# Optimization experiments

Hardware: AMD Instinct MI355X
Metric: run time of the kernel (lower is better)

## Reference

```python
import jax, jax.numpy as jnp
import numpy as np

N = 100000   # num_nodes
E = 800000   # num_edges
D = 128      # dim_in == dim_hidden
DA = 8       # dim_atten
DE = 64      # dim_encoding
DM = D + DE  # mlp hidden (192)
B = 65536    # edge_batch size
NH = 101     # heuristic embedding vocab
SLOPE = 0.2  # leaky_relu negative slope
EPS = 1e-15


def _gtm_att(x, row, col, wr, wc, wx, bx):
    # edge-wise multiplicative attention + sparse softmax + sparse matmul reduce
    ar = x @ wr.T                                   # [N, DA]
    ac = x @ wc.T                                   # [N, DA]
    s = jnp.sum(ar[row] * ac[col], axis=1) * (1.0 / np.sqrt(DA))  # [E]
    s = jnp.where(s >= 0, s, SLOPE * s)             # leaky_relu
    s = jnp.exp(s - jnp.max(s))
    denom = jax.ops.segment_sum(s, row, num_segments=N)           # [N]
    a = s * (1.0 / (denom + EPS))[row]              # row-normalized attention [E]
    out = jax.ops.segment_sum(a[:, None] * x[col], row, num_segments=N)  # [N, D]
    return out @ wx.T + bx


def _gtm(x, row, col, wres, bres, wr, wc, wx, bx, wo, bo):
    y = (x @ wres.T + bres) + _gtm_att(x, row, col, wr, wc, wx, bx)
    return y @ wo.T + bo


def _layernorm(h, g, b):
    mu = jnp.mean(h, axis=-1, keepdims=True)
    var = jnp.var(h, axis=-1, keepdims=True)
    return (h - mu) / jnp.sqrt(var + 1e-5) * g + b


def _forward(x, l0_wres, l0_bres, l0_wr, l0_wc, l0_wx, l0_bx, l0_wo, l0_bo,
             l1_wres, l1_bres, l1_wr, l1_wc, l1_wx, l1_bx, l1_wo, l1_bo,
             emb_h, mlp0_w, mlp0_b, mlp1_w, mlp1_b, ln_g, ln_b,
             f0_w, f0_b, f1_w, f1_b, row, col, eb_src, eb_dst, eb_h):
    h = _gtm(x, row, col, l0_wres, l0_bres, l0_wr, l0_wc, l0_wx, l0_bx, l0_wo, l0_bo)
    h = jax.nn.relu(h)
    h = _gtm(h, row, col, l1_wres, l1_bres, l1_wr, l1_wc, l1_wx, l1_bx, l1_wo, l1_bo)
    z = h[eb_src] * h[eb_dst]                       # [B, D] hadamard link feature
    z = jnp.concatenate([z, emb_h[eb_h]], axis=1)   # [B, DM]
    for w, b in ((mlp0_w, mlp0_b), (mlp1_w, mlp1_b)):
        z = jax.nn.relu(_layernorm(z @ w.T + b, ln_g, ln_b))
    z = z @ f0_w.T + f0_b
    z = z @ f1_w.T + f1_b
    return jax.nn.sigmoid(z)                        # [B, 1]


def setup_inputs() -> dict:
    key = jax.random.key(0)
    ks = jax.random.split(key, 40)
    it = iter(range(40))
    def rn(shape, scale=1.0):
        return jax.random.normal(ks[next(it)], shape, jnp.float32) * scale
    def ri(shape, hi):
        return jax.random.randint(ks[next(it)], shape, 0, hi)
    s_d = 1.0 / np.sqrt(D)
    s_m = 1.0 / np.sqrt(DM)
    inp = {
        "x": rn((N, D)),
        "row": jnp.sort(ri((E,), N)),
        "col": ri((E,), N),
        "eb_src": ri((B,), N),
        "eb_dst": ri((B,), N),
        "eb_h": ri((B,), NH),
    }
    for l in ("l0", "l1"):
        inp[l + "_wres"] = rn((D, D), s_d)
        inp[l + "_bres"] = jnp.zeros((D,), jnp.float32)
        inp[l + "_wr"] = rn((DA, D), s_d)
        inp[l + "_wc"] = rn((DA, D), s_d)
        inp[l + "_wx"] = rn((D, D), s_d)
        inp[l + "_bx"] = jnp.zeros((D,), jnp.float32)
        inp[l + "_wo"] = rn((D, D), s_d)
        inp[l + "_bo"] = jnp.zeros((D,), jnp.float32)
    inp["emb_h"] = rn((NH, DE), 0.1)
    inp["mlp0_w"] = rn((DM, DM), s_m)
    inp["mlp0_b"] = jnp.zeros((DM,), jnp.float32)
    inp["mlp1_w"] = rn((DM, DM), s_m)
    inp["mlp1_b"] = jnp.zeros((DM,), jnp.float32)
    inp["ln_g"] = jnp.ones((DM,), jnp.float32)
    inp["ln_b"] = jnp.zeros((DM,), jnp.float32)
    inp["f0_w"] = rn((64, DM), s_m)
    inp["f0_b"] = jnp.zeros((64,), jnp.float32)
    inp["f1_w"] = rn((1, 64), 0.125)
    inp["f1_b"] = jnp.zeros((1,), jnp.float32)
    return inp


def reference(x, row, col, eb_src, eb_dst, eb_h,
              l0_wres, l0_bres, l0_wr, l0_wc, l0_wx, l0_bx, l0_wo, l0_bo,
              l1_wres, l1_bres, l1_wr, l1_wc, l1_wx, l1_bx, l1_wo, l1_bo,
              emb_h, mlp0_w, mlp0_b, mlp1_w, mlp1_b, ln_g, ln_b,
              f0_w, f0_b, f1_w, f1_b):
    return _forward(x, l0_wres, l0_bres, l0_wr, l0_wc, l0_wx, l0_bx, l0_wo, l0_bo,
                    l1_wres, l1_bres, l1_wr, l1_wc, l1_wx, l1_bx, l1_wo, l1_bo,
                    emb_h, mlp0_w, mlp0_b, mlp1_w, mlp1_b, ln_g, ln_b,
                    f0_w, f0_b, f1_w, f1_b, row, col, eb_src, eb_dst, eb_h)
```

## Files before the change

### kernel.cpp

```cpp
#include <hip/hip_runtime.h>
#include <math.h>

#define D   128
#define DA  8
#define DE  64
#define DMH 192

typedef unsigned short u16;
typedef unsigned int   u32;
typedef __attribute__((ext_vector_type(8))) short bfrag;
typedef __attribute__((ext_vector_type(4))) float facc;

__device__ inline u16 f2bf(float v) {
    unsigned u = __float_as_uint(v);
    return (u16)((u + 0x7fffu + ((u >> 16) & 1u)) >> 16);
}
__device__ inline float bf2f(u16 v) { return __uint_as_float((u32)v << 16); }
__device__ inline u32 pack2(float a, float b) {
    return (u32)f2bf(a) | ((u32)f2bf(b) << 16);
}
__device__ inline bfrag bzero() {
    bfrag r;
#pragma unroll
    for (int i = 0; i < 8; ++i) r[i] = 0;
    return r;
}
__device__ inline bfrag afrag16(const u16* wlds, int row, int kb) {
    int off = row * 256 + (((kb >> 3) * 16) ^ ((row & 7) << 4));
    return *(const bfrag*)((const char*)wlds + off);
}
__device__ inline bfrag zfrag16(const u16* wlds, int row, int kb) {
    int off = row * 384 + (((kb >> 3) * 16) ^ ((row & 7) << 4));
    return *(const bfrag*)((const char*)wlds + off);
}
__device__ inline void st_swz(u16* wlds, int row, int col, int stride, float v) {
    *(u16*)((char*)wlds + row * stride
            + ((((col >> 3) * 16) ^ ((row & 7) << 4)) + (col & 7) * 2)) = f2bf(v);
}
__device__ inline void stage32k(u16* __restrict__ dst, const u16* __restrict__ src,
                                int t) {
    bfrag tmp[8];
#pragma unroll
    for (int i = 0; i < 8; ++i)
        tmp[i] = *(const bfrag*)(src + (size_t)((i << 8) + t) * 8);
#pragma unroll
    for (int i = 0; i < 8; ++i)
        *(bfrag*)(dst + ((i << 8) + t) * 8) = tmp[i];
}

struct PrepSrc { const float* p[14]; };
__global__ __launch_bounds__(256) void prep_all(
    PrepSrc ps, u16* __restrict__ wb,
    const float* __restrict__ x, u16* __restrict__ xb, long n8,
    const int* __restrict__ row, int* __restrict__ rowptr, int E, int N)
{
    long task = (long)blockIdx.x * 256 + threadIdx.x;
    if (task < 194880) {
        int idx = (int)task;
        const int roff[13] = {0, 16384, 32768, 49152, 65536, 81920, 98304,
                              135168, 172032, 184320, 186368, 188416, 194880};
        int r = 0;
#pragma unroll
        for (int k = 1; k < 12; ++k) if (idx >= roff[k]) r = k;
        int local = idx - roff[r];
        float v;
        if (r == 11) {
            v = ps.p[13][local];
        } else {
            int K   = (r >= 6 && r <= 8) ? DMH : D;
            int nks = K >> 5;
            int m = local & 7, lane = (local >> 3) & 63;
            int l16 = lane & 15, lg = lane >> 4;
            int rest = local >> 9;
            int ks = rest % nks, tct = rest / nks;
            int rrow = tct * 16 + l16;
            int k = ks * 32 + lg * 8 + m;
            if (r == 9)       v = (rrow < 8) ? ps.p[9][rrow * D + k]
                                             : ps.p[10][(rrow - 8) * D + k];
            else if (r == 10) v = (rrow < 8) ? ps.p[11][rrow * D + k]
                                             : ps.p[12][(rrow - 8) * D + k];
            else              v = ps.p[r][(size_t)rrow * K + k];
        }
        wb[idx] = f2bf(v);
        return;
    }
    task -= 194880;
    if (task < n8) {
        long i = task;
        __align__(16) float buf[8];
        const float4* p = (const float4*)(x + i * 8);
        ((float4*)buf)[0] = p[0];
        ((float4*)buf)[1] = p[1];
        bfrag o;
#pragma unroll
        for (int k = 0; k < 8; ++k) o[k] = (short)f2bf(buf[k]);
        *(bfrag*)(xb + i * 8) = o;
        return;
    }
    task -= n8;
    if (task < E) {
        int e = (int)task;
        int cur  = row[e];
        int prev = (e == 0) ? -1 : row[e - 1];
        for (int r2 = prev + 1; r2 <= cur; ++r2) rowptr[r2] = e;
        if (e == E - 1)
            for (int r2 = cur + 1; r2 <= N; ++r2) rowptr[r2] = E;
    }
}

__global__ __launch_bounds__(256) void calc_arac(
    const u16* __restrict__ Xb, const u16* __restrict__ wrc,
    float* __restrict__ ar, float* __restrict__ ac, int N)
{
    const int t = threadIdx.x;
    const int w = t >> 6, l = t & 63, l16 = l & 15, lg = l >> 4;
    const long r0 = (long)blockIdx.x * 64 + w * 16;
    const long ia = r0 + l16;
    bfrag a[4];
#pragma unroll
    for (int ks = 0; ks < 4; ++ks)
        a[ks] = (ia < N) ? *(const bfrag*)(Xb + ia * D + ks * 32 + lg * 8) : bzero();
    facc acc = (facc){0, 0, 0, 0};
#pragma unroll
    for (int ks = 0; ks < 4; ++ks) {
        bfrag b = *(const bfrag*)(wrc + ((ks * 64 + l) << 3));
        acc = __builtin_amdgcn_mfma_f32_16x16x32_bf16(a[ks], b, acc, 0, 0, 0);
    }
#pragma unroll
    for (int j = 0; j < 4; ++j) {
        long i = r0 + lg * 4 + j;
        if (i < N) {
            if (l16 < 8) ar[i * DA + l16] = acc[j];
            else         ac[i * DA + (l16 - 8)] = acc[j];
        }
    }
}

__global__ void edge_score(const int* __restrict__ row, const int* __restrict__ col,
                           const float* __restrict__ ar, const float* __restrict__ ac,
                           float* __restrict__ sbuf, int E)
{
    int e = blockIdx.x * 256 + threadIdx.x;
    if (e >= E) return;
    int r = row[e], c = col[e];
    float4 a0 = *(const float4*)&ar[(long)r * DA];
    float4 a1 = *(const float4*)&ar[(long)r * DA + 4];
    float4 c0 = *(const float4*)&ac[(long)c * DA];
    float4 c1 = *(const float4*)&ac[(long)c * DA + 4];
    float s = a0.x * c0.x + a0.y * c0.y + a0.z * c0.z + a0.w * c0.w
            + a1.x * c1.x + a1.y * c1.y + a1.z * c1.z + a1.w * c1.w;
    s *= 0.35355339059327373f;
    s = (s >= 0.f) ? s : 0.2f * s;
    sbuf[e] = expf(s);
}

__global__ __launch_bounds__(256) void aggregate_b(
    const int* __restrict__ rowptr, const int* __restrict__ col,
    const float* __restrict__ sbuf, const u32* __restrict__ Xb2,
    u32* __restrict__ aggb2, int N)
{
    const int w = threadIdx.x >> 6, l = threadIdx.x & 63;
    const int n = blockIdx.x * 4 + w;
    if (n >= N) return;
    const int e0 = rowptr[n], e1 = rowptr[n + 1];
    float p0 = 0.f, p1 = 0.f, ds = 0.f;
    int e = e0;
    for (; e + 8 <= e1; e += 8) {
        float ss[8]; u32 uu[8];
#pragma unroll
        for (int k = 0; k < 8; ++k) {
            int c = col[e + k];
            ss[k] = sbuf[e + k];
            uu[k] = Xb2[((u32)c << 6) + l];
        }
#pragma unroll
        for (int k = 0; k < 8; ++k) {
            ds += ss[k];
            p0 += ss[k] * __uint_as_float(uu[k] << 16);
            p1 += ss[k] * __uint_as_float(uu[k] & 0xffff0000u);
        }
    }
    if (e + 4 <= e1) {
        float ss[4]; u32 uu[4];
#pragma unroll
        for (int k = 0; k < 4; ++k) {
            int c = col[e + k];
            ss[k] = sbuf[e + k];
            uu[k] = Xb2[((u32)c << 6) + l];
        }
#pragma unroll
        for (int k = 0; k < 4; ++k) {
            ds += ss[k];
            p0 += ss[k] * __uint_as_float(uu[k] << 16);
            p1 += ss[k] * __uint_as_float(uu[k] & 0xffff0000u);
        }
        e += 4;
    }
    {
        int rem = e1 - e;
        if (rem > 0) {
            float sa = sbuf[e];
            u32   ua = Xb2[((u32)col[e] << 6) + l];
            float sb = 0.f; u32 ub = 0;
            float sc2 = 0.f; u32 uc = 0;
            if (rem > 1) { sb  = sbuf[e + 1]; ub = Xb2[((u32)col[e + 1] << 6) + l]; }
            if (rem > 2) { sc2 = sbuf[e + 2]; uc = Xb2[((u32)col[e + 2] << 6) + l]; }
            ds += sa + sb + sc2;
            p0 += sa * __uint_as_float(ua << 16);
            p1 += sa * __uint_as_float(ua & 0xffff0000u);
            p0 += sb * __uint_as_float(ub << 16);
            p1 += sb * __uint_as_float(ub & 0xffff0000u);
            p0 += sc2 * __uint_as_float(uc << 16);
            p1 += sc2 * __uint_as_float(uc & 0xffff0000u);
        }
    }
    float sc = 1.f / (ds + 1e-15f);
    aggb2[((u32)n << 6) + l] = pack2(p0 * sc, p1 * sc);
}

template<bool RELU, bool ARAC>
__global__ __launch_bounds__(256) void gtm_fused16(
    const u16* __restrict__ Xb, const u16* __restrict__ aggb,
    const u16* __restrict__ wres, const float* __restrict__ bres,
    const u16* __restrict__ wx, const float* __restrict__ bx,
    const u16* __restrict__ wo, const float* __restrict__ bo,
    const u16* __restrict__ wrc_next, float* __restrict__ ar,
    float* __restrict__ ac, u16* __restrict__ hb, int N)
{
    __shared__ u16 wsh[16384];
    __shared__ u16 ylds4[4][16 * D];
    const int t = threadIdx.x;
    const int w = t >> 6, l = t & 63, l16 = l & 15, lg = l >> 4;
    u16* ylds = ylds4[w];
    const long r0 = (long)blockIdx.x * 64 + w * 16;
    const long ia = r0 + l16;

    bfrag xa[4], ga[4];
#pragma unroll
    for (int ks = 0; ks < 4; ++ks) {
        if (ia < N) {
            xa[ks] = *(const bfrag*)(Xb   + ia * D + ks * 32 + lg * 8);
            ga[ks] = *(const bfrag*)(aggb + ia * D + ks * 32 + lg * 8);
        } else { xa[ks] = bzero(); ga[ks] = bzero(); }
    }

    facc acc[8];
#pragma unroll
    for (int ct = 0; ct < 8; ++ct) acc[ct] = (facc){0, 0, 0, 0};

    stage32k(wsh, wres, t);
    __syncthreads();
#pragma unroll
    for (int ks = 0; ks < 4; ++ks)
#pragma unroll
        for (int ct = 0; ct < 8; ++ct) {
            bfrag b = *(const bfrag*)(wsh + (((ct * 4 + ks) * 64 + l) << 3));
            acc[ct] = __builtin_amdgcn_mfma_f32_16x16x32_bf16(xa[ks], b, acc[ct], 0, 0, 0);
        }
    __syncthreads();

    stage32k(wsh, wx, t);
    __syncthreads();
#pragma unroll
    for (int ks = 0; ks < 4; ++ks)
#pragma unroll
        for (int ct = 0; ct < 8; ++ct) {
            bfrag b = *(const bfrag*)(wsh + (((ct * 4 + ks) * 64 + l) << 3));
            acc[ct] = __builtin_amdgcn_mfma_f32_16x16x32_bf16(ga[ks], b, acc[ct], 0, 0, 0);
        }
    __syncthreads();

    stage32k(wsh, wo, t);
#pragma unroll
    for (int ct = 0; ct < 8; ++ct) {
        int col = ct * 16 + l16;
        float bsum = bres[col] + bx[col];
#pragma unroll
        for (int j = 0; j < 4; ++j)
            st_swz(ylds, lg * 4 + j, col, 256, acc[ct][j] + bsum);
    }
    __syncthreads();

#pragma unroll
    for (int ct = 0; ct < 8; ++ct) acc[ct] = (facc){0, 0, 0, 0};
#pragma unroll
    for (int ks = 0; ks < 4; ++ks) {
        bfrag a = afrag16(ylds, l16, ks * 32 + lg * 8);
#pragma unroll
        for (int ct = 0; ct < 8; ++ct) {
            bfrag b = *(const bfrag*)(wsh + (((ct * 4 + ks) * 64 + l) << 3));
            acc[ct] = __builtin_amdgcn_mfma_f32_16x16x32_bf16(a, b, acc[ct], 0, 0, 0);
        }
    }
    asm volatile("s_waitcnt lgkmcnt(0)" ::: "memory");
    __builtin_amdgcn_sched_barrier(0);
#pragma unroll
    for (int ct = 0; ct < 8; ++ct) {
        int col = ct * 16 + l16;
        float bov = bo[col];
#pragma unroll
        for (int j = 0; j < 4; ++j) {
            long i = r0 + lg * 4 + j;
            float y = acc[ct][j] + bov;
            if (RELU) y = fmaxf(y, 0.f);
            if (i < N) hb[i * D + col] = f2bf(y);
            if (ARAC) st_swz(ylds, lg * 4 + j, col, 256, y);
        }
    }
    if (ARAC) {
        asm volatile("s_waitcnt lgkmcnt(0)" ::: "memory");
        __builtin_amdgcn_sched_barrier(0);
        facc pr = (facc){0, 0, 0, 0};
#pragma unroll
        for (int ks = 0; ks < 4; ++ks) {
            bfrag b = *(const bfrag*)(wrc_next + ((ks * 64 + l) << 3));
            bfrag a = afrag16(ylds, l16, ks * 32 + lg * 8);
            pr = __builtin_amdgcn_mfma_f32_16x16x32_bf16(a, b, pr, 0, 0, 0);
        }
#pragma unroll
        for (int j = 0; j < 4; ++j) {
            long i = r0 + lg * 4 + j;
            if (i < N) {
                if (l16 < 8) ar[i * DA + l16] = pr[j];
                else         ac[i * DA + (l16 - 8)] = pr[j];
            }
        }
    }
}

__device__ inline void ln_relu_to_lds(facc acc[12], const float* __restrict__ bb,
                                      const float* __restrict__ g,
                                      const float* __restrict__ bln,
                                      int l16, int lg, u16* wz)
{
    float s1[4] = {0, 0, 0, 0}, s2[4] = {0, 0, 0, 0};
#pragma unroll
    for (int ct = 0; ct < 12; ++ct) {
        float bbv = bb[ct * 16 + l16];
#pragma unroll
        for (int j = 0; j < 4; ++j) {
            float xv = acc[ct][j] + bbv;
            acc[ct][j] = xv;
            s1[j] += xv; s2[j] += xv * xv;
        }
    }
#pragma unroll
    for (int j = 0; j < 4; ++j) {
#pragma unroll
        for (int off = 1; off < 16; off <<= 1) {
            s1[j] += __shfl_xor(s1[j], off);
            s2[j] += __shfl_xor(s2[j], off);
        }
    }
#pragma unroll
    for (int ct = 0; ct < 12; ++ct) {
        int cc = ct * 16 + l16;
        float gv = g[cc], bv = bln[cc];
#pragma unroll
        for (int j = 0; j < 4; ++j) {
            float mu  = s1[j] * (1.f / 192.f);
            float var = s2[j] * (1.f / 192.f) - mu * mu;
            float y = (acc[ct][j] - mu) * rsqrtf(var + 1e-5f) * gv + bv;
            y = fmaxf(y, 0.f);
            st_swz(wz, lg * 4 + j, cc, 384, y);
        }
    }
    asm volatile("s_waitcnt lgkmcnt(0)" ::: "memory");
    __builtin_amdgcn_sched_barrier(0);
}

__global__ __launch_bounds__(256) void mlp_tail4(
    const u16* __restrict__ hb,
    const int* __restrict__ src, const int* __restrict__ dst,
    const int* __restrict__ ebh, const u16* __restrict__ embb,
    const u16* __restrict__ w0, const float* __restrict__ b0,
    const u16* __restrict__ w1, const float* __restrict__ b1,
    const float* __restrict__ g, const float* __restrict__ bln,
    const u16* __restrict__ f0w, const float* __restrict__ f0b,
    const float* __restrict__ f1w, const float* __restrict__ f1b,
    float* __restrict__ out, int B)
{
    __shared__ u16 wst[18432];
    __shared__ u16 zs[4][16 * DMH];
    const int t = threadIdx.x;
    const int w = t >> 6, l = t & 63, l16 = l & 15, lg = l >> 4;
    u16* wz = zs[w];
    const long r0 = (long)blockIdx.x * 64 + w * 16;
    const long ri = r0 + l16;

    bfrag za[6];
    if (ri < B) {
        int si = src[ri], di = dst[ri], hi2 = ebh[ri];
#pragma unroll
        for (int ks = 0; ks < 4; ++ks) {
            bfrag hs = *(const bfrag*)(hb + (size_t)si * D + ks * 32 + lg * 8);
            bfrag hd = *(const bfrag*)(hb + (size_t)di * D + ks * 32 + lg * 8);
            bfrag r;
#pragma unroll
            for (int k = 0; k < 8; ++k)
                r[k] = (short)f2bf(bf2f((u16)hs[k]) * bf2f((u16)hd[k]));
            za[ks] = r;
        }
        za[4] = *(const bfrag*)(embb + (size_t)hi2 * DE + lg * 8);
        za[5] = *(const bfrag*)(embb + (size_t)hi2 * DE + 32 + lg * 8);
    } else {
#pragma unroll
        for (int ks = 0; ks < 6; ++ks) za[ks] = bzero();
    }

    facc acc[12];
#pragma unroll
    for (int ct = 0; ct < 12; ++ct) acc[ct] = (facc){0, 0, 0, 0};
#pragma unroll
    for (int c = 0; c < 2; ++c) {
        {
            bfrag tmp[9];
#pragma unroll
            for (int i = 0; i < 9; ++i)
                tmp[i] = *(const bfrag*)(w0 + (size_t)c * 18432 + ((i * 256 + t) << 3));
#pragma unroll
            for (int i = 0; i < 9; ++i)
                *(bfrag*)(wst + ((i * 256 + t) << 3)) = tmp[i];
        }
        __syncthreads();
#pragma unroll
        for (int ks = 0; ks < 6; ++ks)
#pragma unroll
            for (int ctl = 0; ctl < 6; ++ctl) {
                bfrag b = *(const bfrag*)(wst + (((ctl * 6 + ks) * 64 + l) << 3));
                acc[c * 6 + ctl] =
                    __builtin_amdgcn_mfma_f32_16x16x32_bf16(za[ks], b, acc[c * 6 + ctl], 0, 0, 0);
            }
        __syncthreads();
    }
    ln_relu_to_lds(acc, b0, g, bln, l16, lg, wz);

#pragma unroll
    for (int ct = 0; ct < 12; ++ct) acc[ct] = (facc){0, 0, 0, 0};
#pragma unroll
    for (int c = 0; c < 2; ++c) {
        {
            bfrag tmp[9];
#pragma unroll
            for (int i = 0; i < 9; ++i)
                tmp[i] = *(const bfrag*)(w1 + (size_t)c * 18432 + ((i * 256 + t) << 3));
#pragma unroll
            for (int i = 0; i < 9; ++i)
                *(bfrag*)(wst + ((i * 256 + t) << 3)) = tmp[i];
        }
        __syncthreads();
#pragma unroll
        for (int ks = 0; ks < 6; ++ks) {
            bfrag a = zfrag16(wz, l16, ks * 32 + lg * 8);
#pragma unroll
            for (int ctl = 0; ctl < 6; ++ctl) {
                bfrag b = *(const bfrag*)(wst + (((ctl * 6 + ks) * 64 + l) << 3));
                acc[c * 6 + ctl] =
                    __builtin_amdgcn_mfma_f32_16x16x32_bf16(a, b, acc[c * 6 + ctl], 0, 0, 0);
            }
        }
        __syncthreads();
    }
    ln_relu_to_lds(acc, b1, g, bln, l16, lg, wz);

    {
        bfrag tmp[6];
#pragma unroll
        for (int i = 0; i < 6; ++i)
            tmp[i] = *(const bfrag*)(f0w + ((i * 256 + t) << 3));
#pragma unroll
        for (int i = 0; i < 6; ++i)
            *(bfrag*)(wst + ((i * 256 + t) << 3)) = tmp[i];
    }
    __syncthreads();
    facc o[4];
#pragma unroll
    for (int ct = 0; ct < 4; ++ct) o[ct] = (facc){0, 0, 0, 0};
#pragma unroll
    for (int ks = 0; ks < 6; ++ks) {
        bfrag a = zfrag16(wz, l16, ks * 32 + lg * 8);
#pragma unroll
        for (int ct = 0; ct < 4; ++ct) {
            bfrag b = *(const bfrag*)(wst + (((ct * 6 + ks) * 64 + l) << 3));
            o[ct] = __builtin_amdgcn_mfma_f32_16x16x32_bf16(a, b, o[ct], 0, 0, 0);
        }
    }
    float p[4] = {0, 0, 0, 0};
#pragma unroll
    for (int ct = 0; ct < 4; ++ct) {
        int cc = ct * 16 + l16;
        float fb = f0b[cc], fw = f1w[cc];
#pragma unroll
        for (int j = 0; j < 4; ++j) p[j] += (o[ct][j] + fb) * fw;
    }
#pragma unroll
    for (int j = 0; j < 4; ++j) {
#pragma unroll
        for (int off = 1; off < 16; off <<= 1) p[j] += __shfl_xor(p[j], off);
    }
    if (l16 == 0) {
#pragma unroll
        for (int j = 0; j < 4; ++j) {
            long i = r0 + lg * 4 + j;
            if (i < B) out[i] = 1.f / (1.f + expf(-(p[j] + f1b[0])));
        }
    }
}

extern "C" void kernel_launch(void* const* d_in, const int* in_sizes, int n_in,
                              void* d_out, int out_size, void* d_ws, size_t ws_size,
                              hipStream_t stream)
{
    const float* x      = (const float*)d_in[0];
    const int*   row    = (const int*)d_in[1];
    const int*   col    = (const int*)d_in[2];
    const int*   eb_src = (const int*)d_in[3];
    const int*   eb_dst = (const int*)d_in[4];
    const int*   eb_h   = (const int*)d_in[5];
    const float* l_wres[2] = {(const float*)d_in[6],  (const float*)d_in[14]};
    const float* l_bres[2] = {(const float*)d_in[7],  (const float*)d_in[15]};
    const float* l_wr[2]   = {(const float*)d_in[8],  (const float*)d_in[16]};
    const float* l_wc[2]   = {(const float*)d_in[9],  (const float*)d_in[17]};
    const float* l_wx[2]   = {(const float*)d_in[10], (const float*)d_in[18]};
    const float* l_bx[2]   = {(const float*)d_in[11], (const float*)d_in[19]};
    const float* l_wo[2]   = {(const float*)d_in[12], (const float*)d_in[20]};
    const float* l_bo[2]   = {(const float*)d_in[13], (const float*)d_in[21]};
    const float* emb_h  = (const float*)d_in[22];
    const float* mlp0_w = (const float*)d_in[23];
    const float* mlp0_b = (const float*)d_in[24];
    const float* mlp1_w = (const float*)d_in[25];
    const float* mlp1_b = (const float*)d_in[26];
    const float* ln_g   = (const float*)d_in[27];
    const float* ln_b   = (const float*)d_in[28];
    const float* f0_w   = (const float*)d_in[29];
    const float* f0_b   = (const float*)d_in[30];
    const float* f1_w   = (const float*)d_in[31];
    const float* f1_b   = (const float*)d_in[32];

    const int N = in_sizes[0] / D;
    const int E = in_sizes[1];
    const int B = in_sizes[3];

    float* arb  = (float*)d_ws;
    float* acb  = arb + (size_t)N * DA;
    float* sbuf = acb + (size_t)N * DA;
    int* rowptr = (int*)(sbuf + (size_t)E);
    uintptr_t bp = (uintptr_t)(rowptr + (N + 1));
    bp = (bp + 15) & ~(uintptr_t)15;
    u16* xb   = (u16*)bp;
    u16* h0b  = xb  + (size_t)N * D;
    u16* hfb  = h0b + (size_t)N * D;
    u16* aggb = hfb + (size_t)N * D;
    u16* WB   = aggb + (size_t)N * D;

    const u16* WRES[2] = {WB + 0,     WB + 49152};
    const u16* WX[2]   = {WB + 16384, WB + 65536};
    const u16* WO[2]   = {WB + 32768, WB + 81920};
    const u16* MW0  = WB + 98304;
    const u16* MW1  = WB + 135168;
    const u16* F0W  = WB + 172032;
    const u16* WRC[2] = {WB + 184320, WB + 186368};
    const u16* EMBB = WB + 188416;

    PrepSrc ps;
    ps.p[0] = l_wres[0]; ps.p[1] = l_wx[0]; ps.p[2] = l_wo[0];
    ps.p[3] = l_wres[1]; ps.p[4] = l_wx[1]; ps.p[5] = l_wo[1];
    ps.p[6] = mlp0_w;    ps.p[7] = mlp1_w;  ps.p[8] = f0_w;
    ps.p[9] = l_wr[0];   ps.p[10] = l_wc[0];
    ps.p[11] = l_wr[1];  ps.p[12] = l_wc[1];
    ps.p[13] = emb_h;

    const int nb64  = (N + 63) / 64;
    const int nbN4  = (N + 3) / 4;
    const int nbE   = (E + 255) / 256;
    const int nbB64 = (B + 63) / 64;
    const long n8   = (long)N * D / 8;
    const long T    = 194880 + n8 + (long)E;
    const int nbT   = (int)((T + 255) / 256);

    prep_all<<<nbT, 256, 0, stream>>>(ps, WB, x, xb, n8, row, rowptr, E, N);
    calc_arac<<<nb64, 256, 0, stream>>>(xb, WRC[0], arb, acb, N);

    edge_score<<<nbE, 256, 0, stream>>>(row, col, arb, acb, sbuf, E);
    aggregate_b<<<nbN4, 256, 0, stream>>>(rowptr, col, sbuf,
                                          (const u32*)xb, (u32*)aggb, N);
    gtm_fused16<true, true><<<nb64, 256, 0, stream>>>(
        xb, aggb, WRES[0], l_bres[0], WX[0], l_bx[0],
        WO[0], l_bo[0], WRC[1], arb, acb, h0b, N);

    edge_score<<<nbE, 256, 0, stream>>>(row, col, arb, acb, sbuf, E);
    aggregate_b<<<nbN4, 256, 0, stream>>>(rowptr, col, sbuf,
                                          (const u32*)h0b, (u32*)aggb, N);
    gtm_fused16<false, false><<<nb64, 256, 0, stream>>>(
        h0b, aggb, WRES[1], l_bres[1], WX[1], l_bx[1],
        WO[1], l_bo[1], nullptr, nullptr, nullptr, hfb, N);

    mlp_tail4<<<nbB64, 256, 0, stream>>>(
        hfb, eb_src, eb_dst, eb_h, EMBB,
        MW0, mlp0_b, MW1, mlp1_b, ln_g, ln_b,
        F0W, f0_b, f1_w, f1_b, (float*)d_out, B);
}
```

Before: 239.6 us.

## Prefetch next weight chunk into registers during MFMA compute in GTM and MLP kernels

Weight staging is software-pipelined: the next weight tile is loaded from global memory into registers while the current tile in LDS feeds the MFMA loop. After that loop it is written to LDS. This hides global load latency behind compute in both the GTM fused kernel and the link MLP kernel. In exchange, register pressure rises (8-9 extra bfrag per thread), which may lower occupancy, and the synchronisation order gets more intricate.

```diff
diff --git a/kernel.cpp b/kernel.cpp
--- a/kernel.cpp
+++ b/kernel.cpp
@@ -37,15 +37,25 @@
     *(u16*)((char*)wlds + row * stride
             + ((((col >> 3) * 16) ^ ((row & 7) << 4)) + (col & 7) * 2)) = f2bf(v);
 }
-__device__ inline void stage32k(u16* __restrict__ dst, const u16* __restrict__ src,
-                                int t) {
-    bfrag tmp[8];
+__device__ inline void ldw8(bfrag* r, const u16* __restrict__ src, int t) {
 #pragma unroll
     for (int i = 0; i < 8; ++i)
-        tmp[i] = *(const bfrag*)(src + (size_t)((i << 8) + t) * 8);
+        r[i] = *(const bfrag*)(src + (size_t)((i << 8) + t) * 8);
+}
+__device__ inline void stw8(u16* __restrict__ dst, const bfrag* r, int t) {
 #pragma unroll
     for (int i = 0; i < 8; ++i)
-        *(bfrag*)(dst + ((i << 8) + t) * 8) = tmp[i];
+        *(bfrag*)(dst + ((i << 8) + t) * 8) = r[i];
+}
+__device__ inline void ldw9(bfrag* r, const u16* __restrict__ src, int t) {
+#pragma unroll
+    for (int i = 0; i < 9; ++i)
+        r[i] = *(const bfrag*)(src + (size_t)((i * 256 + t) << 3));
+}
+__device__ inline void stw9(u16* __restrict__ dst, const bfrag* r, int t) {
+#pragma unroll
+    for (int i = 0; i < 9; ++i)
+        *(bfrag*)(dst + ((i * 256 + t) << 3)) = r[i];
 }
 
 struct PrepSrc { const float* p[14]; };
@@ -235,6 +245,9 @@
     const long r0 = (long)blockIdx.x * 64 + w * 16;
     const long ia = r0 + l16;
 
+    bfrag wreg[8];
+    ldw8(wreg, wres, t);
+
     bfrag xa[4], ga[4];
 #pragma unroll
     for (int ks = 0; ks < 4; ++ks) {
@@ -248,8 +261,9 @@
 #pragma unroll
     for (int ct = 0; ct < 8; ++ct) acc[ct] = (facc){0, 0, 0, 0};
 
-    stage32k(wsh, wres, t);
-    __syncthreads();
+    stw8(wsh, wreg, t);
+    __syncthreads();
+    ldw8(wreg, wx, t);
 #pragma unroll
     for (int ks = 0; ks < 4; ++ks)
 #pragma unroll
@@ -259,8 +273,9 @@
         }
     __syncthreads();
 
-    stage32k(wsh, wx, t);
-    __syncthreads();
+    stw8(wsh, wreg, t);
+    __syncthreads();
+    ldw8(wreg, wo, t);
 #pragma unroll
     for (int ks = 0; ks < 4; ++ks)
 #pragma unroll
@@ -270,7 +285,7 @@
         }
     __syncthreads();
 
-    stage32k(wsh, wo, t);
+    stw8(wsh, wreg, t);
 #pragma unroll
     for (int ct = 0; ct < 8; ++ct) {
         int col = ct * 16 + l16;
@@ -388,6 +403,9 @@
     const long r0 = (long)blockIdx.x * 64 + w * 16;
     const long ri = r0 + l16;
 
+    bfrag wreg[9];
+    ldw9(wreg, w0, t);
+
     bfrag za[6];
     if (ri < B) {
         int si = src[ri], di = dst[ri], hi2 = ebh[ri];
@@ -411,68 +429,69 @@
     facc acc[12];
 #pragma unroll
     for (int ct = 0; ct < 12; ++ct) acc[ct] = (facc){0, 0, 0, 0};
-#pragma unroll
-    for (int c = 0; c < 2; ++c) {
-        {
-            bfrag tmp[9];
-#pragma unroll
-            for (int i = 0; i < 9; ++i)
-                tmp[i] = *(const bfrag*)(w0 + (size_t)c * 18432 + ((i * 256 + t) << 3));
-#pragma unroll
-            for (int i = 0; i < 9; ++i)
-                *(bfrag*)(wst + ((i * 256 + t) << 3)) = tmp[i];
-        }
-        __syncthreads();
-#pragma unroll
-        for (int ks = 0; ks < 6; ++ks)
+    stw9(wst, wreg, t);
+    __syncthreads();
+    ldw9(wreg, w0 + 18432, t);
+#pragma unroll
+    for (int ks = 0; ks < 6; ++ks)
+#pragma unroll
+        for (int ctl = 0; ctl < 6; ++ctl) {
+            bfrag b = *(const bfrag*)(wst + (((ctl * 6 + ks) * 64 + l) << 3));
+            acc[ctl] = __builtin_amdgcn_mfma_f32_16x16x32_bf16(za[ks], b, acc[ctl], 0, 0, 0);
+        }
+    __syncthreads();
+    stw9(wst, wreg, t);
+    __syncthreads();
+    ldw9(wreg, w1, t);
+#pragma unroll
+    for (int ks = 0; ks < 6; ++ks)
+#pragma unroll
+        for (int ctl = 0; ctl < 6; ++ctl) {
+            bfrag b = *(const bfrag*)(wst + (((ctl * 6 + ks) * 64 + l) << 3));
+            acc[6 + ctl] = __builtin_amdgcn_mfma_f32_16x16x32_bf16(za[ks], b, acc[6 + ctl], 0, 0, 0);
+        }
+    ln_relu_to_lds(acc, b0, g, bln, l16, lg, wz);
+    __syncthreads();
+
+#pragma unroll
+    for (int ct = 0; ct < 12; ++ct) acc[ct] = (facc){0, 0, 0, 0};
+    stw9(wst, wreg, t);
+    __syncthreads();
+    ldw9(wreg, w1 + 18432, t);
+#pragma unroll
+    for (int ks = 0; ks < 6; ++ks) {
+        bfrag a = zfrag16(wz, l16, ks * 32 + lg * 8);
+#pragma unroll
+        for (int ctl = 0; ctl < 6; ++ctl) {
+            bfrag b = *(const bfrag*)(wst + (((ctl * 6 + ks) * 64 + l) << 3));
+            acc[ctl] = __builtin_amdgcn_mfma_f32_16x16x32_bf16(a, b, acc[ctl], 0, 0, 0);
+        }
+    }
+    __syncthreads();
+    stw9(wst, wreg, t);
+    __syncthreads();
+    {
+        bfrag f6[6];
+#pragma unroll
+        for (int i = 0; i < 6; ++i)
+            f6[i] = *(const bfrag*)(f0w + ((i * 256 + t) << 3));
+#pragma unroll
+        for (int ks = 0; ks < 6; ++ks) {
+            bfrag a = zfrag16(wz, l16, ks * 32 + lg * 8);
 #pragma unroll
             for (int ctl = 0; ctl < 6; ++ctl) {
                 bfrag b = *(const bfrag*)(wst + (((ctl * 6 + ks) * 64 + l) << 3));
-                acc[c * 6 + ctl] =
-                    __builtin_amdgcn_mfma_f32_16x16x32_bf16(za[ks], b, acc[c * 6 + ctl], 0, 0, 0);
+                acc[6 + ctl] = __builtin_amdgcn_mfma_f32_16x16x32_bf16(a, b, acc[6 + ctl], 0, 0, 0);
             }
+        }
+        ln_relu_to_lds(acc, b1, g, bln, l16, lg, wz);
         __syncthreads();
-    }
-    ln_relu_to_lds(acc, b0, g, bln, l16, lg, wz);
-
-#pragma unroll
-    for (int ct = 0; ct < 12; ++ct) acc[ct] = (facc){0, 0, 0, 0};
-#pragma unroll
-    for (int c = 0; c < 2; ++c) {
-        {
-            bfrag tmp[9];
-#pragma unroll
-            for (int i = 0; i < 9; ++i)
-                tmp[i] = *(const bfrag*)(w1 + (size_t)c * 18432 + ((i * 256 + t) << 3));
-#pragma unroll
-            for (int i = 0; i < 9; ++i)
-                *(bfrag*)(wst + ((i * 256 + t) << 3)) = tmp[i];
-        }
-        __syncthreads();
-#pragma unroll
-        for (int ks = 0; ks < 6; ++ks) {
-            bfrag a = zfrag16(wz, l16, ks * 32 + lg * 8);
-#pragma unroll
-            for (int ctl = 0; ctl < 6; ++ctl) {
-                bfrag b = *(const bfrag*)(wst + (((ctl * 6 + ks) * 64 + l) << 3));
-                acc[c * 6 + ctl] =
-                    __builtin_amdgcn_mfma_f32_16x16x32_bf16(a, b, acc[c * 6 + ctl], 0, 0, 0);
-            }
-        }
-        __syncthreads();
-    }
-    ln_relu_to_lds(acc, b1, g, bln, l16, lg, wz);
-
-    {
-        bfrag tmp[6];
 #pragma unroll
         for (int i = 0; i < 6; ++i)
-            tmp[i] = *(const bfrag*)(f0w + ((i * 256 + t) << 3));
-#pragma unroll
-        for (int i = 0; i < 6; ++i)
-            *(bfrag*)(wst + ((i * 256 + t) << 3)) = tmp[i];
-    }
-    __syncthreads();
+            *(bfrag*)(wst + ((i * 256 + t) << 3)) = f6[i];
+    }
+    __syncthreads();
+
     facc o[4];
 #pragma unroll
     for (int ct = 0; ct < 4; ++ct) o[ct] = (facc){0, 0, 0, 0};
```

Result: slower. 244.6 us (+2.1%).
